# Kernel tuning notes

Hardware: AMD Instinct MI355X
Metric: run time of the kernel (lower is better)

The kernel has to match this reference:

```python
import jax, jax.numpy as jnp
import numpy as np

N_HEAD, D_MODEL, D_HEAD = 16, 1024, 64
BSZ, SEQLEN = 2, 2048
ROPE_BASE = 10000.0


def _rope_tables(seqlen, d_head, base=ROPE_BASE):
    # freqs_cis = exp(i * t * theta_j), theta_j = base^(-2j/d_head)
    inv_freq = 1.0 / (base ** (np.arange(0, d_head, 2, dtype=np.float32) / d_head))
    t = np.arange(seqlen, dtype=np.float32)
    ang = np.outer(t, inv_freq)  # [S, d_head//2]
    return jnp.asarray(np.cos(ang)), jnp.asarray(np.sin(ang))


def setup_inputs() -> dict:
    key = jax.random.key(0)
    ks = jax.random.split(key, 5)
    x = jax.random.normal(ks[0], (BSZ, SEQLEN, D_MODEL), dtype=jnp.float32)
    freqs_cos, freqs_sin = _rope_tables(SEQLEN, D_HEAD)
    scale = 0.02
    # weights stored as (in, out) so projection is x @ w
    wq = jax.random.normal(ks[1], (D_MODEL, N_HEAD * D_HEAD), dtype=jnp.float32) * scale
    wk = jax.random.normal(ks[2], (D_MODEL, N_HEAD * D_HEAD), dtype=jnp.float32) * scale
    wv = jax.random.normal(ks[3], (D_MODEL, N_HEAD * D_HEAD), dtype=jnp.float32) * scale
    wo = jax.random.normal(ks[4], (N_HEAD * D_HEAD, D_MODEL), dtype=jnp.float32) * scale
    return {"x": x, "freqs_cos": freqs_cos, "freqs_sin": freqs_sin,
            "wq": wq, "wk": wk, "wv": wv, "wo": wo}


def _apply_rope(t, cos, sin):
    # t: [B, S, H, Dh]; complex pairs are consecutive elements (x0 + i*x1)
    B, S, H, Dh = t.shape
    tf = t.astype(jnp.float32).reshape(B, S, H, Dh // 2, 2)
    t0, t1 = tf[..., 0], tf[..., 1]
    c = cos[None, :, None, :]  # [1, S, 1, Dh//2]
    s = sin[None, :, None, :]
    o0 = t0 * c - t1 * s
    o1 = t0 * s + t1 * c
    return jnp.stack([o0, o1], axis=-1).reshape(B, S, H, Dh).astype(t.dtype)


def reference(x, freqs_cos, freqs_sin, wq, wk, wv, wo):
    B, S, _ = x.shape
    H, Dh = N_HEAD, D_HEAD
    q = jnp.einsum('bsd,de->bse', x, wq).reshape(B, S, H, Dh)
    k = jnp.einsum('bsd,de->bse', x, wk).reshape(B, S, H, Dh)
    v = jnp.einsum('bsd,de->bse', x, wv).reshape(B, S, H, Dh)
    q = _apply_rope(q, freqs_cos, freqs_sin)
    k = _apply_rope(k, freqs_cos, freqs_sin)
    # [B, H, S, Dh]
    q = q.transpose(0, 2, 1, 3)
    k = k.transpose(0, 2, 1, 3)
    v = v.transpose(0, 2, 1, 3)
    scores = jnp.einsum('bhqd,bhkd->bhqk', q, k) / jnp.sqrt(jnp.float32(Dh))
    probs = jax.nn.softmax(scores.astype(jnp.float32), axis=-1).astype(q.dtype)
    out = jnp.einsum('bhqk,bhkd->bhqd', probs, v)  # [B, H, S, Dh]
    out = out.transpose(0, 2, 1, 3).reshape(B, S, H * Dh)
    return jnp.einsum('bse,ed->bsd', out, wo)
```

## Files before the change

kernel.cpp:

```cpp
#include <hip/hip_runtime.h>
#include <math.h>

#define BSZ 2
#define SEQ 2048
#define NH 16
#define DH 64
#define DM 1024
#define HD 1024

typedef _Float16 h16;
typedef _Float16 half8 __attribute__((ext_vector_type(8)));
typedef _Float16 half4 __attribute__((ext_vector_type(4)));
typedef float f32x4 __attribute__((ext_vector_type(4)));

__device__ __forceinline__ f32x4 mfma16(half8 a, half8 b, f32x4 c) {
    return __builtin_amdgcn_mfma_f32_16x16x32_f16(a, b, c, 0, 0, 0);
}

__device__ __forceinline__ void async_copy16(h16* lds, const h16* g) {
    __builtin_amdgcn_global_load_lds(
        (const __attribute__((address_space(1))) unsigned int*)g,
        (__attribute__((address_space(3))) unsigned int*)lds, 16, 0, 0);
}

#define SWZ(cb, r) ((((cb) ^ ((r) & 7)) * 8))

__global__ __launch_bounds__(256) void cvt_x_kernel(const float* __restrict__ x,
                                                    h16* __restrict__ x16)
{
    int i = (blockIdx.x * 256 + threadIdx.x) * 8;
    float4 a = *(const float4*)&x[i];
    float4 b = *(const float4*)&x[i + 4];
    half8 o;
    o[0] = (h16)a.x; o[1] = (h16)a.y; o[2] = (h16)a.z; o[3] = (h16)a.w;
    o[4] = (h16)b.x; o[5] = (h16)b.y; o[6] = (h16)b.z; o[7] = (h16)b.w;
    *(half8*)&x16[i] = o;
}

__global__ __launch_bounds__(256) void wtrans_kernel(
    const float* __restrict__ wq, const float* __restrict__ wk,
    const float* __restrict__ wv, const float* __restrict__ wo,
    h16* __restrict__ wt)
{
    const float* w = (blockIdx.z == 0) ? wq : (blockIdx.z == 1) ? wk
                   : (blockIdx.z == 2) ? wv : wo;
    h16* ot = wt + (size_t)blockIdx.z * DM * DM;
    __shared__ float tile[64][68];
    const int k0 = blockIdx.y * 64, n0 = blockIdx.x * 64;
    const int t = threadIdx.x;
    const int r = t >> 2, c4 = (t & 3) * 16;
#pragma unroll
    for (int i = 0; i < 16; i += 4) {
        float4 v = *(const float4*)&w[(size_t)(k0 + r) * DM + n0 + c4 + i];
        tile[r][c4 + i + 0] = v.x; tile[r][c4 + i + 1] = v.y;
        tile[r][c4 + i + 2] = v.z; tile[r][c4 + i + 3] = v.w;
    }
    __syncthreads();
#pragma unroll
    for (int g = 0; g < 2; ++g) {
        half8 hh;
#pragma unroll
        for (int j = 0; j < 8; ++j)
            hh[j] = (h16)tile[c4 + g * 8 + j][r];
        *(half8*)&ot[(size_t)(n0 + r) * DM + k0 + c4 + g * 8] = hh;
    }
}

__global__ __launch_bounds__(256) void qkv_kernel(
    const h16* __restrict__ x16, const h16* __restrict__ wt,
    const float* __restrict__ fcos, const float* __restrict__ fsin,
    h16* __restrict__ Q16, h16* __restrict__ K16, h16* __restrict__ VT16)
{
    const int z = blockIdx.z;
    const h16* __restrict__ bw = wt + (size_t)z * DM * DM;

    __shared__ h16 smem[17408];
    h16* As = smem;
    h16* Bs = smem + 8192;
    h16* Vt = smem;

    const int m0 = blockIdx.y * 128;
    const int n0 = blockIdx.x * 128;
    const int t  = threadIdx.x;
    const int w  = t >> 6, ln = t & 63;
    const int L  = ln & 15, U = ln >> 4;
    const int wm = (w >> 1) * 64, wn = (w & 1) * 64;

    const int sr  = ln >> 3;
    const int scb = (ln & 7) ^ sr;

    f32x4 acc[4][4];
#pragma unroll
    for (int i = 0; i < 4; ++i)
#pragma unroll
        for (int j = 0; j < 4; ++j) acc[i][j] = (f32x4)0.0f;

    for (int k0 = 0; k0 < DM; k0 += 64) {
        __syncthreads();
#pragma unroll
        for (int c = 0; c < 4; ++c) {
            int rb = w * 32 + c * 8;
            async_copy16(&As[rb * 64], &x16[(size_t)(m0 + rb + sr) * DM + k0 + scb * 8]);
            async_copy16(&Bs[rb * 64], &bw [(size_t)(n0 + rb + sr) * DM + k0 + scb * 8]);
        }
        __syncthreads();

#pragma unroll
        for (int ks = 0; ks < 2; ++ks) {
            half8 af[4], bf[4];
#pragma unroll
            for (int mt = 0; mt < 4; ++mt)
                af[mt] = *(const half8*)&As[(wm + mt * 16 + L) * 64 + SWZ(ks * 4 + U, L)];
#pragma unroll
            for (int nt = 0; nt < 4; ++nt)
                bf[nt] = *(const half8*)&Bs[(wn + nt * 16 + L) * 64 + SWZ(ks * 4 + U, L)];
#pragma unroll
            for (int mt = 0; mt < 4; ++mt)
#pragma unroll
                for (int nt = 0; nt < 4; ++nt)
                    acc[mt][nt] = mfma16(bf[nt], af[mt], acc[mt][nt]);
        }
    }

    const int b = m0 >> 11;
    const int sbase = m0 & 2047;

    if (z < 2) {
        const float sc = (z == 0) ? 0.125f * 1.44269504088896f : 1.0f;
#pragma unroll
        for (int mt = 0; mt < 4; ++mt) {
            int s = sbase + wm + mt * 16 + L;
            const float* ct = &fcos[s * 32];
            const float* st = &fsin[s * 32];
#pragma unroll
            for (int nt = 0; nt < 4; ++nt) {
                int nl = n0 + wn + nt * 16 + U * 4;
                int d = nl & 63, h = nl >> 6;
                int pd = d >> 1;
                float cv0 = ct[pd], sv0 = st[pd];
                float cv1 = ct[pd + 1], sv1 = st[pd + 1];
                float v0 = acc[mt][nt][0], v1 = acc[mt][nt][1];
                float v2 = acc[mt][nt][2], v3 = acc[mt][nt][3];
                float o0 = (v0 * cv0 - v1 * sv0) * sc;
                float o1 = (v0 * sv0 + v1 * cv0) * sc;
                float o2 = (v2 * cv1 - v3 * sv1) * sc;
                float o3 = (v2 * sv1 + v3 * cv1) * sc;
                size_t addr = ((size_t)(b * NH + h) * SEQ + s) * DH + d;
                half4 kk;
                kk[0] = (h16)o0; kk[1] = (h16)o1; kk[2] = (h16)o2; kk[3] = (h16)o3;
                if (z == 0) *(half4*)&Q16[addr] = kk;
                else        *(half4*)&K16[addr] = kk;
            }
        }
    } else {
        __syncthreads();
#pragma unroll
        for (int mt = 0; mt < 4; ++mt)
#pragma unroll
            for (int nt = 0; nt < 4; ++nt)
#pragma unroll
                for (int r = 0; r < 4; ++r) {
                    int nloc = wn + nt * 16 + U * 4 + r;
                    int sloc = wm + mt * 16 + L;
                    Vt[nloc * 136 + sloc] = (h16)acc[mt][nt][r];
                }
        __syncthreads();
#pragma unroll
        for (int i = 0; i < 8; ++i) {
            int c = i * 256 + t;
            int dl = c >> 4;
            int s8 = (c & 15) * 8;
            half8 vv = *(const half8*)&Vt[dl * 136 + s8];
            int n = n0 + dl;
            int d = n & 63, h = n >> 6;
            *(half8*)&VT16[((size_t)(b * NH + h) * DH + d) * SEQ + sbase + s8] = vv;
        }
    }
}

#define LDA 72

__global__ __launch_bounds__(512, 4) void attn_kernel(
    const h16* __restrict__ Q16, const h16* __restrict__ K16,
    const h16* __restrict__ VT16, h16* __restrict__ A16)
{
    __shared__ h16 Ks[64 * 64];
    __shared__ h16 VTs[64 * 64];
    __shared__ h16 Ps[128 * LDA];

    const int t = threadIdx.x, w = t >> 6, ln = t & 63;
    const int L = ln & 15, U = ln >> 4;
    const int q0 = blockIdx.x * 128;
    const int bh = blockIdx.y;
    const size_t base = (size_t)bh * SEQ * DH;

    half8 qf[2];
#pragma unroll
    for (int ks = 0; ks < 2; ++ks)
        qf[ks] = *(const half8*)&Q16[base + (size_t)(q0 + w * 16 + L) * DH + ks * 32 + U * 8];

    f32x4 O[4];
#pragma unroll
    for (int dt = 0; dt < 4; ++dt) O[dt] = (f32x4)0.0f;
    float m_i = -1e30f, l_i = 0.0f;

    const int sr  = ln >> 3;
    const int scb = (ln & 7) ^ sr;
    const int rb  = w * 8;

    for (int j0 = 0; j0 < SEQ; j0 += 64) {
        __syncthreads();
        async_copy16(&Ks[rb * 64],  &K16 [base + (size_t)(j0 + rb + sr) * DH + scb * 8]);
        async_copy16(&VTs[rb * 64], &VT16[base + (size_t)(rb + sr) * SEQ + j0 + scb * 8]);
        __syncthreads();

        f32x4 S[4];
#pragma unroll
        for (int nt = 0; nt < 4; ++nt) {
            S[nt] = (f32x4)0.0f;
#pragma unroll
            for (int ks = 0; ks < 2; ++ks) {
                half8 kf = *(const half8*)&Ks[(nt * 16 + L) * 64 + SWZ(ks * 4 + U, L)];
                S[nt] = mfma16(kf, qf[ks], S[nt]);
            }
        }

        float mx = -1e30f;
#pragma unroll
        for (int nt = 0; nt < 4; ++nt)
#pragma unroll
            for (int r = 0; r < 4; ++r) mx = fmaxf(mx, S[nt][r]);
        mx = fmaxf(mx, __shfl_xor(mx, 16, 64));
        mx = fmaxf(mx, __shfl_xor(mx, 32, 64));
        float mnew  = fmaxf(m_i, mx);
        float alpha = exp2f(m_i - mnew);
        float rs = 0.0f;
        int prow = (w * 16 + L) * LDA;
#pragma unroll
        for (int nt = 0; nt < 4; ++nt) {
            float p0 = exp2f(S[nt][0] - mnew);
            float p1 = exp2f(S[nt][1] - mnew);
            float p2 = exp2f(S[nt][2] - mnew);
            float p3 = exp2f(S[nt][3] - mnew);
            rs += (p0 + p1) + (p2 + p3);
            half4 pq;
            pq[0] = (h16)p0; pq[1] = (h16)p1; pq[2] = (h16)p2; pq[3] = (h16)p3;
            *(half4*)&Ps[prow + nt * 16 + U * 4] = pq;
        }
        rs += __shfl_xor(rs, 16, 64);
        rs += __shfl_xor(rs, 32, 64);
        m_i = mnew;
        l_i = l_i * alpha + rs;
#pragma unroll
        for (int dt = 0; dt < 4; ++dt) O[dt] *= alpha;

        half8 pf[2];
#pragma unroll
        for (int ks = 0; ks < 2; ++ks)
            pf[ks] = *(const half8*)&Ps[prow + ks * 32 + U * 8];
#pragma unroll
        for (int dt = 0; dt < 4; ++dt)
#pragma unroll
            for (int ks = 0; ks < 2; ++ks) {
                half8 vf = *(const half8*)&VTs[(dt * 16 + L) * 64 + SWZ(ks * 4 + U, L)];
                O[dt] = mfma16(vf, pf[ks], O[dt]);
            }
    }

    const int b = bh >> 4, h = bh & 15;
    float inv = 1.0f / l_i;
    int s = q0 + w * 16 + L;
#pragma unroll
    for (int dt = 0; dt < 4; ++dt) {
        half4 o4;
#pragma unroll
        for (int r = 0; r < 4; ++r) o4[r] = (h16)(O[dt][r] * inv);
        *(half4*)&A16[(size_t)(b * SEQ + s) * HD + h * DH + dt * 16 + U * 4] = o4;
    }
}

__global__ __launch_bounds__(256) void oproj_kernel(
    const h16* __restrict__ A16, const h16* __restrict__ bw,
    float* __restrict__ out)
{
    __shared__ h16 As[128 * 64];
    __shared__ h16 Bs[64 * 64];

    const int m0 = blockIdx.y * 128;
    const int n0 = blockIdx.x * 64;
    const int t  = threadIdx.x;
    const int w  = t >> 6, ln = t & 63;
    const int L  = ln & 15, U = ln >> 4;

    const int sr  = ln >> 3;
    const int scb = (ln & 7) ^ sr;

    f32x4 acc[2][4];
#pragma unroll
    for (int i = 0; i < 2; ++i)
#pragma unroll
        for (int j = 0; j < 4; ++j) acc[i][j] = (f32x4)0.0f;

    for (int k0 = 0; k0 < DM; k0 += 64) {
        __syncthreads();
#pragma unroll
        for (int c = 0; c < 4; ++c) {
            int rb = w * 32 + c * 8;
            async_copy16(&As[rb * 64], &A16[(size_t)(m0 + rb + sr) * DM + k0 + scb * 8]);
        }
#pragma unroll
        for (int c = 0; c < 2; ++c) {
            int rb = w * 16 + c * 8;
            async_copy16(&Bs[rb * 64], &bw[(size_t)(n0 + rb + sr) * DM + k0 + scb * 8]);
        }
        __syncthreads();

#pragma unroll
        for (int ks = 0; ks < 2; ++ks) {
            half8 af[2], bf[4];
#pragma unroll
            for (int mt = 0; mt < 2; ++mt)
                af[mt] = *(const half8*)&As[(w * 32 + mt * 16 + L) * 64 + SWZ(ks * 4 + U, L)];
#pragma unroll
            for (int nt = 0; nt < 4; ++nt)
                bf[nt] = *(const half8*)&Bs[(nt * 16 + L) * 64 + SWZ(ks * 4 + U, L)];
#pragma unroll
            for (int mt = 0; mt < 2; ++mt)
#pragma unroll
                for (int nt = 0; nt < 4; ++nt)
                    acc[mt][nt] = mfma16(af[mt], bf[nt], acc[mt][nt]);
        }
    }

#pragma unroll
    for (int mt = 0; mt < 2; ++mt)
#pragma unroll
        for (int nt = 0; nt < 4; ++nt)
#pragma unroll
            for (int r = 0; r < 4; ++r) {
                int row = m0 + w * 32 + mt * 16 + U * 4 + r;
                int col = n0 + nt * 16 + L;
                out[(size_t)row * DM + col] = acc[mt][nt][r];
            }
}

extern "C" void kernel_launch(void* const* d_in, const int* in_sizes, int n_in,
                              void* d_out, int out_size, void* d_ws, size_t ws_size,
                              hipStream_t stream)
{
    const float* x    = (const float*)d_in[0];
    const float* fcos = (const float*)d_in[1];
    const float* fsin = (const float*)d_in[2];
    const float* wq   = (const float*)d_in[3];
    const float* wk   = (const float*)d_in[4];
    const float* wv   = (const float*)d_in[5];
    const float* wo   = (const float*)d_in[6];
    float* out = (float*)d_out;

    const size_t M4 = (size_t)4 * 1024 * 1024;
    h16* x16  = (h16*)d_ws;
    h16* wt   = x16 + M4;
    h16* Q16  = wt + M4;
    h16* K16  = Q16 + M4;
    h16* VT16 = K16 + M4;
    h16* A16  = VT16 + M4;

    cvt_x_kernel<<<2048, 256, 0, stream>>>(x, x16);
    wtrans_kernel<<<dim3(16, 16, 4), 256, 0, stream>>>(wq, wk, wv, wo, wt);
    qkv_kernel<<<dim3(8, 32, 3), 256, 0, stream>>>(x16, wt, fcos, fsin,
                                                   Q16, K16, VT16);
    attn_kernel<<<dim3(16, 32), 512, 0, stream>>>(Q16, K16, VT16, A16);
    oproj_kernel<<<dim3(16, 32), 256, 0, stream>>>(A16, wt + 3 * (size_t)DM * DM, out);
}
```

Baseline: 224.0 us.

## Double waves per block in projections and split attention KV across wave pairs

The QKV and output projection kernels move to 512 threads per block, with each wave computing a smaller sub-tile, so the same block tile is covered by more waves. The attention kernel now loads 128-key tiles, and each pair of waves splits the keys between them while each wave handles 32 query rows. The two partial softmax states are merged at the end through shared memory. This aims to raise latency hiding and MFMA utilization, at the cost of more LDS, an extra merge step with barriers, and possible register pressure.

```diff
diff --git a/kernel.cpp b/kernel.cpp
--- a/kernel.cpp
+++ b/kernel.cpp
@@ -66,7 +66,7 @@
     }
 }
 
-__global__ __launch_bounds__(256) void qkv_kernel(
+__global__ __launch_bounds__(512, 4) void qkv_kernel(
     const h16* __restrict__ x16, const h16* __restrict__ wt,
     const float* __restrict__ fcos, const float* __restrict__ fsin,
     h16* __restrict__ Q16, h16* __restrict__ K16, h16* __restrict__ VT16)
@@ -84,22 +84,23 @@
     const int t  = threadIdx.x;
     const int w  = t >> 6, ln = t & 63;
     const int L  = ln & 15, U = ln >> 4;
-    const int wm = (w >> 1) * 64, wn = (w & 1) * 64;
+    const int wm = (w & 3) * 32;
+    const int wn = (w >> 2) * 64;
 
     const int sr  = ln >> 3;
     const int scb = (ln & 7) ^ sr;
 
-    f32x4 acc[4][4];
-#pragma unroll
-    for (int i = 0; i < 4; ++i)
+    f32x4 acc[2][4];
+#pragma unroll
+    for (int i = 0; i < 2; ++i)
 #pragma unroll
         for (int j = 0; j < 4; ++j) acc[i][j] = (f32x4)0.0f;
 
     for (int k0 = 0; k0 < DM; k0 += 64) {
         __syncthreads();
 #pragma unroll
-        for (int c = 0; c < 4; ++c) {
-            int rb = w * 32 + c * 8;
+        for (int c = 0; c < 2; ++c) {
+            int rb = w * 16 + c * 8;
             async_copy16(&As[rb * 64], &x16[(size_t)(m0 + rb + sr) * DM + k0 + scb * 8]);
             async_copy16(&Bs[rb * 64], &bw [(size_t)(n0 + rb + sr) * DM + k0 + scb * 8]);
         }
@@ -107,15 +108,15 @@
 
 #pragma unroll
         for (int ks = 0; ks < 2; ++ks) {
-            half8 af[4], bf[4];
-#pragma unroll
-            for (int mt = 0; mt < 4; ++mt)
+            half8 af[2], bf[4];
+#pragma unroll
+            for (int mt = 0; mt < 2; ++mt)
                 af[mt] = *(const half8*)&As[(wm + mt * 16 + L) * 64 + SWZ(ks * 4 + U, L)];
 #pragma unroll
             for (int nt = 0; nt < 4; ++nt)
                 bf[nt] = *(const half8*)&Bs[(wn + nt * 16 + L) * 64 + SWZ(ks * 4 + U, L)];
 #pragma unroll
-            for (int mt = 0; mt < 4; ++mt)
+            for (int mt = 0; mt < 2; ++mt)
 #pragma unroll
                 for (int nt = 0; nt < 4; ++nt)
                     acc[mt][nt] = mfma16(bf[nt], af[mt], acc[mt][nt]);
@@ -128,7 +129,7 @@
     if (z < 2) {
         const float sc = (z == 0) ? 0.125f * 1.44269504088896f : 1.0f;
 #pragma unroll
-        for (int mt = 0; mt < 4; ++mt) {
+        for (int mt = 0; mt < 2; ++mt) {
             int s = sbase + wm + mt * 16 + L;
             const float* ct = &fcos[s * 32];
             const float* st = &fsin[s * 32];
@@ -155,7 +156,7 @@
     } else {
         __syncthreads();
 #pragma unroll
-        for (int mt = 0; mt < 4; ++mt)
+        for (int mt = 0; mt < 2; ++mt)
 #pragma unroll
             for (int nt = 0; nt < 4; ++nt)
 #pragma unroll
@@ -166,8 +167,8 @@
                 }
         __syncthreads();
 #pragma unroll
-        for (int i = 0; i < 8; ++i) {
-            int c = i * 256 + t;
+        for (int i = 0; i < 4; ++i) {
+            int c = i * 512 + t;
             int dl = c >> 4;
             int s8 = (c & 15) * 8;
             half8 vv = *(const half8*)&Vt[dl * 136 + s8];
@@ -178,108 +179,165 @@
     }
 }
 
-#define LDA 72
+#define PLD 136
 
 __global__ __launch_bounds__(512, 4) void attn_kernel(
     const h16* __restrict__ Q16, const h16* __restrict__ K16,
     const h16* __restrict__ VT16, h16* __restrict__ A16)
 {
-    __shared__ h16 Ks[64 * 64];
-    __shared__ h16 VTs[64 * 64];
-    __shared__ h16 Ps[128 * LDA];
+    __shared__ h16 Ks[128 * 64];
+    __shared__ h16 VTs[64 * 128];
+    __shared__ __align__(16) h16 Ps[128 * PLD];
+    __shared__ float mlbuf[8][2][16][2];
+
+    float* Obuf = (float*)Ps;
 
     const int t = threadIdx.x, w = t >> 6, ln = t & 63;
     const int L = ln & 15, U = ln >> 4;
+    const int pair = w >> 1, half = w & 1;
+    const int qw = pair * 32, kh = half * 64;
     const int q0 = blockIdx.x * 128;
     const int bh = blockIdx.y;
     const size_t base = (size_t)bh * SEQ * DH;
 
-    half8 qf[2];
-#pragma unroll
-    for (int ks = 0; ks < 2; ++ks)
-        qf[ks] = *(const half8*)&Q16[base + (size_t)(q0 + w * 16 + L) * DH + ks * 32 + U * 8];
-
-    f32x4 O[4];
-#pragma unroll
-    for (int dt = 0; dt < 4; ++dt) O[dt] = (f32x4)0.0f;
-    float m_i = -1e30f, l_i = 0.0f;
+    half8 qf[2][2];
+#pragma unroll
+    for (int qb = 0; qb < 2; ++qb)
+#pragma unroll
+        for (int ks = 0; ks < 2; ++ks)
+            qf[qb][ks] = *(const half8*)&Q16[base + (size_t)(q0 + qw + qb * 16 + L) * DH + ks * 32 + U * 8];
+
+    f32x4 O[4][2];
+#pragma unroll
+    for (int dt = 0; dt < 4; ++dt)
+#pragma unroll
+        for (int qb = 0; qb < 2; ++qb) O[dt][qb] = (f32x4)0.0f;
+    float m_i[2] = {-1e30f, -1e30f}, l_i[2] = {0.0f, 0.0f};
 
     const int sr  = ln >> 3;
     const int scb = (ln & 7) ^ sr;
-    const int rb  = w * 8;
-
-    for (int j0 = 0; j0 < SEQ; j0 += 64) {
-        __syncthreads();
-        async_copy16(&Ks[rb * 64],  &K16 [base + (size_t)(j0 + rb + sr) * DH + scb * 8]);
-        async_copy16(&VTs[rb * 64], &VT16[base + (size_t)(rb + sr) * SEQ + j0 + scb * 8]);
-        __syncthreads();
-
-        f32x4 S[4];
+
+    for (int j0 = 0; j0 < SEQ; j0 += 128) {
+        __syncthreads();
+#pragma unroll
+        for (int c = 0; c < 2; ++c) {
+            int rbk = c * 64 + w * 8;
+            async_copy16(&Ks[rbk * 64], &K16[base + (size_t)(j0 + rbk + sr) * DH + scb * 8]);
+        }
+#pragma unroll
+        for (int c = 0; c < 2; ++c) {
+            int rv = (w * 2 + c) * 4;
+            int c16 = (ln & 15) ^ ((rv + U) & 15);
+            async_copy16(&VTs[rv * 128], &VT16[base + (size_t)(rv + U) * SEQ + j0 + c16 * 8]);
+        }
+        __syncthreads();
+
+        f32x4 S[4][2];
 #pragma unroll
         for (int nt = 0; nt < 4; ++nt) {
-            S[nt] = (f32x4)0.0f;
+            S[nt][0] = (f32x4)0.0f;
+            S[nt][1] = (f32x4)0.0f;
 #pragma unroll
             for (int ks = 0; ks < 2; ++ks) {
-                half8 kf = *(const half8*)&Ks[(nt * 16 + L) * 64 + SWZ(ks * 4 + U, L)];
-                S[nt] = mfma16(kf, qf[ks], S[nt]);
+                half8 kf = *(const half8*)&Ks[(kh + nt * 16 + L) * 64 + SWZ(ks * 4 + U, L)];
+                S[nt][0] = mfma16(kf, qf[0][ks], S[nt][0]);
+                S[nt][1] = mfma16(kf, qf[1][ks], S[nt][1]);
             }
         }
 
-        float mx = -1e30f;
-#pragma unroll
-        for (int nt = 0; nt < 4; ++nt)
-#pragma unroll
-            for (int r = 0; r < 4; ++r) mx = fmaxf(mx, S[nt][r]);
-        mx = fmaxf(mx, __shfl_xor(mx, 16, 64));
-        mx = fmaxf(mx, __shfl_xor(mx, 32, 64));
-        float mnew  = fmaxf(m_i, mx);
-        float alpha = exp2f(m_i - mnew);
-        float rs = 0.0f;
-        int prow = (w * 16 + L) * LDA;
-#pragma unroll
-        for (int nt = 0; nt < 4; ++nt) {
-            float p0 = exp2f(S[nt][0] - mnew);
-            float p1 = exp2f(S[nt][1] - mnew);
-            float p2 = exp2f(S[nt][2] - mnew);
-            float p3 = exp2f(S[nt][3] - mnew);
-            rs += (p0 + p1) + (p2 + p3);
-            half4 pq;
-            pq[0] = (h16)p0; pq[1] = (h16)p1; pq[2] = (h16)p2; pq[3] = (h16)p3;
-            *(half4*)&Ps[prow + nt * 16 + U * 4] = pq;
-        }
-        rs += __shfl_xor(rs, 16, 64);
-        rs += __shfl_xor(rs, 32, 64);
-        m_i = mnew;
-        l_i = l_i * alpha + rs;
-#pragma unroll
-        for (int dt = 0; dt < 4; ++dt) O[dt] *= alpha;
-
-        half8 pf[2];
-#pragma unroll
-        for (int ks = 0; ks < 2; ++ks)
-            pf[ks] = *(const half8*)&Ps[prow + ks * 32 + U * 8];
+#pragma unroll
+        for (int qb = 0; qb < 2; ++qb) {
+            float mx = -1e30f;
+#pragma unroll
+            for (int nt = 0; nt < 4; ++nt)
+#pragma unroll
+                for (int r = 0; r < 4; ++r) mx = fmaxf(mx, S[nt][qb][r]);
+            mx = fmaxf(mx, __shfl_xor(mx, 16, 64));
+            mx = fmaxf(mx, __shfl_xor(mx, 32, 64));
+            float mnew  = fmaxf(m_i[qb], mx);
+            float alpha = exp2f(m_i[qb] - mnew);
+            float rs = 0.0f;
+            int prow = (qw + qb * 16 + L) * PLD + kh;
+#pragma unroll
+            for (int nt = 0; nt < 4; ++nt) {
+                float p0 = exp2f(S[nt][qb][0] - mnew);
+                float p1 = exp2f(S[nt][qb][1] - mnew);
+                float p2 = exp2f(S[nt][qb][2] - mnew);
+                float p3 = exp2f(S[nt][qb][3] - mnew);
+                rs += (p0 + p1) + (p2 + p3);
+                half4 pq;
+                pq[0] = (h16)p0; pq[1] = (h16)p1; pq[2] = (h16)p2; pq[3] = (h16)p3;
+                *(half4*)&Ps[prow + nt * 16 + U * 4] = pq;
+            }
+            rs += __shfl_xor(rs, 16, 64);
+            rs += __shfl_xor(rs, 32, 64);
+            m_i[qb] = mnew;
+            l_i[qb] = l_i[qb] * alpha + rs;
+#pragma unroll
+            for (int dt = 0; dt < 4; ++dt) O[dt][qb] *= alpha;
+        }
+
+        half8 pf[2][2];
+#pragma unroll
+        for (int qb = 0; qb < 2; ++qb)
+#pragma unroll
+            for (int ks2 = 0; ks2 < 2; ++ks2)
+                pf[qb][ks2] = *(const half8*)&Ps[(qw + qb * 16 + L) * PLD + kh + ks2 * 32 + U * 8];
 #pragma unroll
         for (int dt = 0; dt < 4; ++dt)
 #pragma unroll
-            for (int ks = 0; ks < 2; ++ks) {
-                half8 vf = *(const half8*)&VTs[(dt * 16 + L) * 64 + SWZ(ks * 4 + U, L)];
-                O[dt] = mfma16(vf, pf[ks], O[dt]);
+            for (int ks2 = 0; ks2 < 2; ++ks2) {
+                half8 vf = *(const half8*)&VTs[(dt * 16 + L) * 128 + ((half * 8 + ks2 * 4 + U) ^ L) * 8];
+                O[dt][0] = mfma16(vf, pf[0][ks2], O[dt][0]);
+                O[dt][1] = mfma16(vf, pf[1][ks2], O[dt][1]);
             }
     }
 
-    const int b = bh >> 4, h = bh & 15;
-    float inv = 1.0f / l_i;
-    int s = q0 + w * 16 + L;
-#pragma unroll
-    for (int dt = 0; dt < 4; ++dt) {
-        half4 o4;
-#pragma unroll
-        for (int r = 0; r < 4; ++r) o4[r] = (h16)(O[dt][r] * inv);
-        *(half4*)&A16[(size_t)(b * SEQ + s) * HD + h * DH + dt * 16 + U * 4] = o4;
-    }
-}
-
-__global__ __launch_bounds__(256) void oproj_kernel(
+    if (U == 0) {
+        mlbuf[w][0][L][0] = m_i[0]; mlbuf[w][0][L][1] = l_i[0];
+        mlbuf[w][1][L][0] = m_i[1]; mlbuf[w][1][L][1] = l_i[1];
+    }
+    __syncthreads();
+    const int pw = w ^ 1;
+    float l_tot[2];
+#pragma unroll
+    for (int qb = 0; qb < 2; ++qb) {
+        float mp = mlbuf[pw][qb][L][0], lp = mlbuf[pw][qb][L][1];
+        float m  = fmaxf(m_i[qb], mp);
+        float ss = exp2f(m_i[qb] - m);
+        float sp = exp2f(mp - m);
+        l_tot[qb] = l_i[qb] * ss + lp * sp;
+#pragma unroll
+        for (int dt = 0; dt < 4; ++dt) O[dt][qb] *= ss;
+    }
+    if (half) {
+#pragma unroll
+        for (int qb = 0; qb < 2; ++qb)
+#pragma unroll
+            for (int dt = 0; dt < 4; ++dt)
+                *(f32x4*)&Obuf[(qw + qb * 16 + L) * 68 + dt * 16 + U * 4] = O[dt][qb];
+    }
+    __syncthreads();
+    if (!half) {
+        const int b = bh >> 4, hh = bh & 15;
+#pragma unroll
+        for (int qb = 0; qb < 2; ++qb) {
+            float inv = 1.0f / l_tot[qb];
+            int s = q0 + qw + qb * 16 + L;
+#pragma unroll
+            for (int dt = 0; dt < 4; ++dt) {
+                f32x4 op = *(const f32x4*)&Obuf[(qw + qb * 16 + L) * 68 + dt * 16 + U * 4];
+                half4 o4;
+#pragma unroll
+                for (int r = 0; r < 4; ++r)
+                    o4[r] = (h16)((O[dt][qb][r] + op[r]) * inv);
+                *(half4*)&A16[(size_t)(b * SEQ + s) * HD + hh * DH + dt * 16 + U * 4] = o4;
+            }
+        }
+    }
+}
+
+__global__ __launch_bounds__(512, 4) void oproj_kernel(
     const h16* __restrict__ A16, const h16* __restrict__ bw,
     float* __restrict__ out)
 {
@@ -295,53 +353,44 @@
     const int sr  = ln >> 3;
     const int scb = (ln & 7) ^ sr;
 
-    f32x4 acc[2][4];
-#pragma unroll
-    for (int i = 0; i < 2; ++i)
-#pragma unroll
-        for (int j = 0; j < 4; ++j) acc[i][j] = (f32x4)0.0f;
+    f32x4 acc[4];
+#pragma unroll
+    for (int j = 0; j < 4; ++j) acc[j] = (f32x4)0.0f;
 
     for (int k0 = 0; k0 < DM; k0 += 64) {
         __syncthreads();
-#pragma unroll
-        for (int c = 0; c < 4; ++c) {
-            int rb = w * 32 + c * 8;
-            async_copy16(&As[rb * 64], &A16[(size_t)(m0 + rb + sr) * DM + k0 + scb * 8]);
-        }
 #pragma unroll
         for (int c = 0; c < 2; ++c) {
             int rb = w * 16 + c * 8;
+            async_copy16(&As[rb * 64], &A16[(size_t)(m0 + rb + sr) * DM + k0 + scb * 8]);
+        }
+        {
+            int rb = w * 8;
             async_copy16(&Bs[rb * 64], &bw[(size_t)(n0 + rb + sr) * DM + k0 + scb * 8]);
         }
         __syncthreads();
 
 #pragma unroll
         for (int ks = 0; ks < 2; ++ks) {
-            half8 af[2], bf[4];
-#pragma unroll
-            for (int mt = 0; mt < 2; ++mt)
-                af[mt] = *(const half8*)&As[(w * 32 + mt * 16 + L) * 64 + SWZ(ks * 4 + U, L)];
+            half8 af, bf[4];
+            af = *(const half8*)&As[(w * 16 + L) * 64 + SWZ(ks * 4 + U, L)];
 #pragma unroll
             for (int nt = 0; nt < 4; ++nt)
                 bf[nt] = *(const half8*)&Bs[(nt * 16 + L) * 64 + SWZ(ks * 4 + U, L)];
 #pragma unroll
-            for (int mt = 0; mt < 2; ++mt)
-#pragma unroll
-                for (int nt = 0; nt < 4; ++nt)
-                    acc[mt][nt] = mfma16(af[mt], bf[nt], acc[mt][nt]);
-        }
-    }
-
-#pragma unroll
-    for (int mt = 0; mt < 2; ++mt)
-#pragma unroll
-        for (int nt = 0; nt < 4; ++nt)
-#pragma unroll
-            for (int r = 0; r < 4; ++r) {
-                int row = m0 + w * 32 + mt * 16 + U * 4 + r;
-                int col = n0 + nt * 16 + L;
-                out[(size_t)row * DM + col] = acc[mt][nt][r];
-            }
+            for (int nt = 0; nt < 4; ++nt)
+                acc[nt] = mfma16(af, bf[nt], acc[nt]);
+        }
+    }
+
+#pragma unroll
+    for (int nt = 0; nt < 4; ++nt)
+#pragma unroll
+        for (int r = 0; r < 4; ++r) {
+            int row = m0 + w * 16 + U * 4 + r;
+            int col = n0 + nt * 16 + L;
+            out[(size_t)row * DM + col] = acc[nt][r];
+        }
 }
 
 extern "C" void kernel_launch(void* const* d_in, const int* in_sizes, int n_in,
@@ -367,8 +416,8 @@
 
     cvt_x_kernel<<<2048, 256, 0, stream>>>(x, x16);
     wtrans_kernel<<<dim3(16, 16, 4), 256, 0, stream>>>(wq, wk, wv, wo, wt);
-    qkv_kernel<<<dim3(8, 32, 3), 256, 0, stream>>>(x16, wt, fcos, fsin,
+    qkv_kernel<<<dim3(8, 32, 3), 512, 0, stream>>>(x16, wt, fcos, fsin,
                                                    Q16, K16, VT16);
     attn_kernel<<<dim3(16, 32), 512, 0, stream>>>(Q16, K16, VT16, A16);
-    oproj_kernel<<<dim3(16, 32), 256, 0, stream>>>(A16, wt + 3 * (size_t)DM * DM, out);
-}
+    oproj_kernel<<<dim3(16, 32), 512, 0, stream>>>(A16, wt + 3 * (size_t)DM * DM, out);
+}
```

Result: faster. 218.0 us (-2.7%).
